# Optimization experiments

Hardware: AMD Instinct MI355X
Metric: run time of the kernel (lower is better)

## Reference

```python
import jax, jax.numpy as jnp
import numpy as np

HEADS = 16
DIM_HEAD = 64
QUERY_DIM = 1024
CONTEXT_DIM = 768
INNER = HEADS * DIM_HEAD  # 1024
SCALE = DIM_HEAD ** -0.5


def setup_inputs() -> dict:
    key = jax.random.key(0)
    ks = jax.random.split(key, 7)
    B, Sq, Skv = 4, 2048, 2048
    x = jax.random.normal(ks[0], (B, Sq, QUERY_DIM), dtype=jnp.float32)
    context = jax.random.normal(ks[1], (B, Skv, CONTEXT_DIM), dtype=jnp.float32)
    # Linear weights stored as (in, out) so y = x @ W
    w_q = jax.random.normal(ks[2], (QUERY_DIM, INNER), dtype=jnp.float32) / np.sqrt(QUERY_DIM)
    w_k = jax.random.normal(ks[3], (CONTEXT_DIM, INNER), dtype=jnp.float32) / np.sqrt(CONTEXT_DIM)
    w_v = jax.random.normal(ks[4], (CONTEXT_DIM, INNER), dtype=jnp.float32) / np.sqrt(CONTEXT_DIM)
    w_o = jax.random.normal(ks[5], (INNER, QUERY_DIM), dtype=jnp.float32) / np.sqrt(INNER)
    b_o = jax.random.normal(ks[6], (QUERY_DIM,), dtype=jnp.float32) * 0.02
    return {"x": x, "context": context, "w_q": w_q, "w_k": w_k, "w_v": w_v, "w_o": w_o, "b_o": b_o}


def reference(x, context, w_q, w_k, w_v, w_o, b_o):
    B, Sq, _ = x.shape
    Skv = context.shape[1]
    # projections, split heads: [B, S, H, D] -> [B, H, S, D]
    q = (x @ w_q).reshape(B, Sq, HEADS, DIM_HEAD).transpose(0, 2, 1, 3)
    k = (context @ w_k).reshape(B, Skv, HEADS, DIM_HEAD).transpose(0, 2, 1, 3)
    v = (context @ w_v).reshape(B, Skv, HEADS, DIM_HEAD).transpose(0, 2, 1, 3)
    sim = jnp.einsum('bhid,bhjd->bhij', q, k) * SCALE
    attn = jax.nn.softmax(sim, axis=-1)
    out = jnp.einsum('bhij,bhjd->bhid', attn, v)
    out = out.transpose(0, 2, 1, 3).reshape(B, Sq, INNER)
    return out @ w_o + b_o
```

## Files before the change

kernel.cpp:

```cpp
#include <hip/hip_runtime.h>

typedef __bf16 bf16_t;
typedef __bf16 bf16x8 __attribute__((ext_vector_type(8)));
typedef __bf16 bf16x4 __attribute__((ext_vector_type(4)));
typedef __bf16 bf16x2 __attribute__((ext_vector_type(2)));
typedef float  f32x4  __attribute__((ext_vector_type(4)));
typedef float  f32x16 __attribute__((ext_vector_type(16)));
typedef int    i32x4  __attribute__((ext_vector_type(4)));

#define AS_G(p) ((const __attribute__((address_space(1))) void*)(p))
#define AS_L(p) ((__attribute__((address_space(3))) void*)(p))
#define GLD16(g, l) __builtin_amdgcn_global_load_lds(AS_G(g), AS_L(l), 16, 0, 0)

static __device__ __forceinline__ f32x4 mfma16(bf16x8 a, bf16x8 b, f32x4 c) {
  return __builtin_amdgcn_mfma_f32_16x16x32_bf16(a, b, c, 0, 0, 0);
}
static __device__ __forceinline__ f32x16 mfma32(bf16x8 a, bf16x8 b, f32x16 c) {
  return __builtin_amdgcn_mfma_f32_32x32x16_bf16(a, b, c, 0, 0, 0);
}
static __device__ __forceinline__ int pk2(float a, float b) {
  bf16x2 t; t[0] = (bf16_t)a; t[1] = (bf16_t)b;
  return __builtin_bit_cast(int, t);
}
static __device__ __forceinline__ bf16x8 mk8(int a, int b, int c, int d) {
  i32x4 v{a, b, c, d};
  return __builtin_bit_cast(bf16x8, v);
}
static __device__ __forceinline__ void pl32swap(int& x, int& y) {
  asm volatile("v_permlane32_swap_b32 %0, %1" : "+v"(x), "+v"(y));
}

__global__ __launch_bounds__(256) void cvt_all_k(const float* __restrict__ x,
                                                 bf16_t* __restrict__ xb,
                                                 const float* __restrict__ ctx,
                                                 bf16_t* __restrict__ cb,
                                                 long nx, long ntot) {
  long i = ((long)blockIdx.x * 256 + threadIdx.x) * 4;
  long step = (long)gridDim.x * 256 * 4;
  for (; i < ntot; i += step) {
    const float* src; bf16_t* dst; long off;
    if (i < nx) { src = x; dst = xb; off = i; }
    else        { src = ctx; dst = cb; off = i - nx; }
    float4 v = *(const float4*)(src + off);
    bf16x4 o;
    o[0] = (bf16_t)v.x; o[1] = (bf16_t)v.y; o[2] = (bf16_t)v.z; o[3] = (bf16_t)v.w;
    *(bf16x4*)(dst + off) = o;
  }
}

__global__ __launch_bounds__(256) void tcvt_all_k(
    const float* __restrict__ w0, const float* __restrict__ w1,
    const float* __restrict__ w2, const float* __restrict__ w3,
    bf16_t* __restrict__ t0, bf16_t* __restrict__ t1,
    bf16_t* __restrict__ t2, bf16_t* __restrict__ t3) {
  __shared__ float t[32][33];
  const int z = blockIdx.z;
  const float* W = (z == 0) ? w0 : (z == 1) ? w1 : (z == 2) ? w2 : w3;
  bf16_t* Wt = (z == 0) ? t0 : (z == 1) ? t1 : (z == 2) ? t2 : t3;
  const int K = (z == 1 || z == 2) ? 768 : 1024;
  const int N = 1024;
  int k0 = blockIdx.y << 5, n0 = blockIdx.x << 5;
  if (k0 >= K) return;
  int ti = threadIdx.x >> 3, tj = (threadIdx.x & 7) << 2;
  float4 v = *(const float4*)(W + (size_t)(k0 + ti) * N + n0 + tj);
  t[ti][tj] = v.x; t[ti][tj + 1] = v.y; t[ti][tj + 2] = v.z; t[ti][tj + 3] = v.w;
  __syncthreads();
  bf16x4 o;
  o[0] = (bf16_t)t[tj + 0][ti]; o[1] = (bf16_t)t[tj + 1][ti];
  o[2] = (bf16_t)t[tj + 2][ti]; o[3] = (bf16_t)t[tj + 3][ti];
  *(bf16x4*)(Wt + (size_t)(n0 + ti) * K + k0 + tj) = o;
}

template <int MODE>
__global__ __launch_bounds__(256, 3) void gemm_bt_k(
    const bf16_t* __restrict__ A, const bf16_t* __restrict__ Bt,
    void* __restrict__ Cout, void* __restrict__ Cout2,
    const float* __restrict__ bias, int N, int K, float oscale) {
  __shared__ __align__(16) char lA[16384];
  __shared__ __align__(16) char lB[16384];
  const int tid = threadIdx.x;
  const int lane = tid & 63;
  const int w = tid >> 6;
  const int wr = (w >> 1) << 6;
  const int wc = (w & 1) << 6;
  const long row0 = (long)blockIdx.x << 7;
  const long col0 = (long)blockIdx.y << 7;

  const int r_st = tid >> 3;
  const int cb_st = ((tid & 7) << 4) ^ ((r_st & 7) << 4);
  const char* pa = (const char*)(A + (row0 + r_st) * (long)K) + cb_st;
  const char* pb = (const char*)(Bt + (col0 + r_st) * (long)K) + cb_st;
  const long rowstep = (long)K * 64;
  char* la = lA + tid * 16;
  char* lb = lB + tid * 16;

  f32x4 acc[4][4];
#pragma unroll
  for (int m = 0; m < 4; m++)
#pragma unroll
    for (int n = 0; n < 4; n++) acc[m][n] = f32x4{0.f, 0.f, 0.f, 0.f};

  for (int k0 = 0; k0 < K; k0 += 64) {
    __syncthreads();
#pragma unroll
    for (int i = 0; i < 4; i++) {
      GLD16(pa + i * rowstep, la + i * 4096);
      GLD16(pb + i * rowstep, lb + i * 4096);
    }
    __syncthreads();
    pa += 128; pb += 128;
#pragma unroll
    for (int ks = 0; ks < 2; ks++) {
      bf16x8 af[4], bfr[4];
#pragma unroll
      for (int m = 0; m < 4; m++) {
        int row = wr + (m << 4) + (lane & 15);
        int cby = ((ks << 6) + ((lane >> 4) << 4)) ^ ((row & 7) << 4);
        af[m] = *(const bf16x8*)(lA + row * 128 + cby);
      }
#pragma unroll
      for (int n = 0; n < 4; n++) {
        int row = wc + (n << 4) + (lane & 15);
        int cby = ((ks << 6) + ((lane >> 4) << 4)) ^ ((row & 7) << 4);
        bfr[n] = *(const bf16x8*)(lB + row * 128 + cby);
      }
      __builtin_amdgcn_s_setprio(1);
#pragma unroll
      for (int m = 0; m < 4; m++)
#pragma unroll
        for (int n = 0; n < 4; n++)
          acc[m][n] = mfma16(af[m], bfr[n], acc[m][n]);
      __builtin_amdgcn_s_setprio(0);
    }
  }

  if (MODE == 0) {
    bf16_t* Cb = (bf16_t*)Cout;
#pragma unroll
    for (int n = 0; n < 4; n++) {
      long c = col0 + wc + (n << 4) + (lane & 15);
      long h = c >> 6, d = c & 63;
#pragma unroll
      for (int m = 0; m < 4; m++) {
#pragma unroll
        for (int j = 0; j < 4; j++) {
          long rr = row0 + wr + (m << 4) + ((lane >> 4) << 2) + j;
          long bb = rr >> 11, s = rr & 2047;
          Cb[(((bb << 4) + h) * 2048 + s) * 64 + d] = (bf16_t)(acc[m][n][j] * oscale);
        }
      }
    }
  } else if (MODE == 1) {
    float* Cf = (float*)Cout;
#pragma unroll
    for (int n = 0; n < 4; n++) {
      long c = col0 + wc + (n << 4) + (lane & 15);
      float bv = bias[c];
#pragma unroll
      for (int m = 0; m < 4; m++) {
#pragma unroll
        for (int j = 0; j < 4; j++) {
          long rr = row0 + wr + (m << 4) + ((lane >> 4) << 2) + j;
          Cf[rr * (long)N + c] = acc[m][n][j] + bv;
        }
      }
    }
  } else {
    if (col0 < 1024) {
      bf16_t* Cb = (bf16_t*)Cout;
#pragma unroll
      for (int n = 0; n < 4; n++) {
        long c = col0 + wc + (n << 4) + (lane & 15);
        long h = c >> 6, d = c & 63;
#pragma unroll
        for (int m = 0; m < 4; m++) {
#pragma unroll
          for (int j = 0; j < 4; j++) {
            long rr = row0 + wr + (m << 4) + ((lane >> 4) << 2) + j;
            long bb = rr >> 11, s = rr & 2047;
            Cb[(((bb << 4) + h) * 2048 + s) * 64 + d] = (bf16_t)acc[m][n][j];
          }
        }
      }
    } else {
      bf16_t* Cb = (bf16_t*)Cout2;
#pragma unroll
      for (int n = 0; n < 4; n++) {
        long c = (col0 - 1024) + wc + (n << 4) + (lane & 15);
        long h = c >> 6, d = c & 63;
#pragma unroll
        for (int m = 0; m < 4; m++) {
          long rr = row0 + wr + (m << 4) + ((lane >> 4) << 2);
          long bb = rr >> 11, s = rr & 2047;
          bf16x4 ov;
#pragma unroll
          for (int j = 0; j < 4; j++) ov[j] = (bf16_t)acc[m][n][j];
          *(bf16x4*)(Cb + (((bb << 4) + h) * 64 + d) * 2048 + s) = ov;
        }
      }
    }
  }
}

__global__ __launch_bounds__(256, 3) void attn5_k(
    const bf16_t* __restrict__ Q, const bf16_t* __restrict__ Kh,
    const bf16_t* __restrict__ VT, bf16_t* __restrict__ O) {
  __shared__ __align__(16) char lds_[32768];
  const int tid = threadIdx.x;
  const int lane = tid & 63;
  const int w = tid >> 6;
  const int hi = lane >> 5;
  const int lq = lane & 31;
  const int bh = blockIdx.x;
  const int b = bh >> 4, hh = bh & 15;
  const int q = (blockIdx.y << 7) + (w << 5) + lq;

  const bf16_t* qp = Q + ((size_t)bh * 2048 + q) * 64 + (hi << 3);
  bf16x8 qf[4];
#pragma unroll
  for (int s = 0; s < 4; s++) qf[s] = *(const bf16x8*)(qp + (s << 4));

  const bf16x8 onesf = mk8(0x3F803F80, 0x3F803F80, 0x3F803F80, 0x3F803F80);

  const int r_st = tid >> 3;
  const int csw = ((tid & 7) << 4) ^ ((r_st & 7) << 4);
  const char* pk = (const char*)Kh + (size_t)bh * 262144 + r_st * 128 + csw;
  const char* pv = (const char*)VT + (size_t)bh * 262144 + (size_t)r_st * 4096 + csw;
  const int swz = (lane & 7) << 4;

  f32x16 oa[2], la;
#pragma unroll
  for (int t = 0; t < 2; t++)
#pragma unroll
    for (int r = 0; r < 16; r++) oa[t][r] = 0.f;
#pragma unroll
  for (int r = 0; r < 16; r++) la[r] = 0.f;

  GLD16(pk, lds_ + tid * 16);
  GLD16(pk + 4096, lds_ + 4096 + tid * 16);
  GLD16(pv, lds_ + 8192 + tid * 16);
  GLD16(pv + 131072, lds_ + 12288 + tid * 16);
  __syncthreads();

  for (int it = 0; it < 32; it++) {
    const int buf = it & 1;
    if (it < 31) {
      const char* pkn = pk + (it + 1) * 8192;
      const char* pvn = pv + (it + 1) * 128;
      char* dst = lds_ + ((buf ^ 1) << 14);
      GLD16(pkn, dst + tid * 16);
      GLD16(pkn + 4096, dst + 4096 + tid * 16);
      GLD16(pvn, dst + 8192 + tid * 16);
      GLD16(pvn + 131072, dst + 12288 + tid * 16);
    }
    const char* lk = lds_ + (buf << 14);
    const char* lv = lk + 8192;

    f32x16 sa[2];
#pragma unroll
    for (int h = 0; h < 2; h++) {
#pragma unroll
      for (int r = 0; r < 16; r++) sa[h][r] = 0.f;
      const char* krow = lk + (((h << 5) + lq) << 7);
      __builtin_amdgcn_s_setprio(1);
#pragma unroll
      for (int s = 0; s < 4; s++) {
        bf16x8 kf = *(const bf16x8*)(krow + (((s << 5) + (hi << 4)) ^ swz));
        sa[h] = mfma32(kf, qf[s], sa[h]);
      }
      __builtin_amdgcn_s_setprio(0);
    }

#pragma unroll
    for (int h = 0; h < 2; h++)
#pragma unroll
      for (int r = 0; r < 16; r++)
        sa[h][r] = __builtin_amdgcn_exp2f(sa[h][r]);

    bf16x8 pf[4];
#pragma unroll
    for (int h = 0; h < 2; h++) {
      int x0 = pk2(sa[h][0], sa[h][1]),   y0 = pk2(sa[h][4], sa[h][5]);
      int x1 = pk2(sa[h][2], sa[h][3]),   y1 = pk2(sa[h][6], sa[h][7]);
      pl32swap(x0, y0); pl32swap(x1, y1);
      pf[h * 2 + 0] = mk8(x0, x1, y0, y1);
      int x2 = pk2(sa[h][8], sa[h][9]),   y2 = pk2(sa[h][12], sa[h][13]);
      int x3 = pk2(sa[h][10], sa[h][11]), y3 = pk2(sa[h][14], sa[h][15]);
      pl32swap(x2, y2); pl32swap(x3, y3);
      pf[h * 2 + 1] = mk8(x2, x3, y2, y3);
    }

    __builtin_amdgcn_s_setprio(1);
#pragma unroll
    for (int t = 0; t < 2; t++) {
      const char* vrw = lv + (((t << 5) + lq) << 7);
#pragma unroll
      for (int s = 0; s < 4; s++) {
        bf16x8 vf = *(const bf16x8*)(vrw + (((s << 5) + (hi << 4)) ^ swz));
        oa[t] = mfma32(vf, pf[s], oa[t]);
      }
    }
#pragma unroll
    for (int s = 0; s < 4; s++) la = mfma32(onesf, pf[s], la);
    __builtin_amdgcn_s_setprio(0);
    __syncthreads();
  }

  float invl = 1.f / la[0];
  bf16_t* Ob = O + ((size_t)b * 2048 + q) * 1024 + hh * 64;
#pragma unroll
  for (int t = 0; t < 2; t++)
#pragma unroll
    for (int g = 0; g < 4; g++) {
      bf16x4 ov;
#pragma unroll
      for (int j = 0; j < 4; j++) ov[j] = (bf16_t)(oa[t][(g << 2) + j] * invl);
      *(bf16x4*)(Ob + (t << 5) + (g << 3) + (hi << 2)) = ov;
    }
}

extern "C" void kernel_launch(void* const* d_in, const int* in_sizes, int n_in,
                              void* d_out, int out_size, void* d_ws, size_t ws_size,
                              hipStream_t stream) {
  (void)in_sizes; (void)n_in; (void)out_size; (void)ws_size;
  const float* x   = (const float*)d_in[0];
  const float* ctx = (const float*)d_in[1];
  const float* w_q = (const float*)d_in[2];
  const float* w_k = (const float*)d_in[3];
  const float* w_v = (const float*)d_in[4];
  const float* w_o = (const float*)d_in[5];
  const float* b_o = (const float*)d_in[6];

  char* ws = (char*)d_ws;
  const size_t MB = 1 << 20;
  bf16_t* xb  = (bf16_t*)(ws);
  bf16_t* cb  = (bf16_t*)(ws + 16 * MB);
  bf16_t* wqT = (bf16_t*)(ws + 28 * MB);
  bf16_t* wkT = (bf16_t*)(ws + 30 * MB);
  bf16_t* wvT = (bf16_t*)(ws + 31 * MB + 512 * 1024);
  bf16_t* woT = (bf16_t*)(ws + 33 * MB);
  bf16_t* qws = (bf16_t*)(ws + 35 * MB);
  bf16_t* kws = (bf16_t*)(ws + 51 * MB);
  bf16_t* vtw = (bf16_t*)(ws + 67 * MB);
  bf16_t* ows = xb;

  cvt_all_k<<<2048, 256, 0, stream>>>(x, xb, ctx, cb, 8388608L, 14680064L);
  tcvt_all_k<<<dim3(32, 32, 4), 256, 0, stream>>>(w_q, w_k, w_v, w_o, wqT, wkT, wvT, woT);

  const float qs = 0.125f * 1.4426950408889634f;
  gemm_bt_k<0><<<dim3(64, 8), 256, 0, stream>>>(xb, wqT, qws, nullptr, nullptr, 1024, 1024, qs);
  gemm_bt_k<3><<<dim3(64, 16), 256, 0, stream>>>(cb, wkT, kws, vtw, nullptr, 2048, 768, 1.0f);
  attn5_k<<<dim3(64, 16), 256, 0, stream>>>(qws, kws, vtw, ows);
  gemm_bt_k<1><<<dim3(64, 8), 256, 0, stream>>>(ows, woT, d_out, nullptr, b_o, 1024, 1024, 1.0f);
}
```

Measured before the change: 172.0 us.

## Fuse fp32-to-bf16 activation conversion into projection GEMM A-tile loads

Removes the standalone conversion kernel for x and context. The Q and KV projection GEMMs now read fp32 activations directly into registers, convert them to bf16 and write them swizzled into LDS, with the next tile prefetched in registers. This saves a kernel launch and a full write and re-read of the bf16 activation copies. In exchange the A operand uses register-staged loads instead of async global-to-LDS loads, which raises register pressure and reads twice the bytes per tile. Under the Q/KV grids each row of x or context is also read and converted once per column block instead of once overall.

```diff
diff --git a/kernel.cpp b/kernel.cpp
--- a/kernel.cpp
+++ b/kernel.cpp
@@ -28,24 +28,6 @@
 }
 static __device__ __forceinline__ void pl32swap(int& x, int& y) {
   asm volatile("v_permlane32_swap_b32 %0, %1" : "+v"(x), "+v"(y));
-}
-
-__global__ __launch_bounds__(256) void cvt_all_k(const float* __restrict__ x,
-                                                 bf16_t* __restrict__ xb,
-                                                 const float* __restrict__ ctx,
-                                                 bf16_t* __restrict__ cb,
-                                                 long nx, long ntot) {
-  long i = ((long)blockIdx.x * 256 + threadIdx.x) * 4;
-  long step = (long)gridDim.x * 256 * 4;
-  for (; i < ntot; i += step) {
-    const float* src; bf16_t* dst; long off;
-    if (i < nx) { src = x; dst = xb; off = i; }
-    else        { src = ctx; dst = cb; off = i - nx; }
-    float4 v = *(const float4*)(src + off);
-    bf16x4 o;
-    o[0] = (bf16_t)v.x; o[1] = (bf16_t)v.y; o[2] = (bf16_t)v.z; o[3] = (bf16_t)v.w;
-    *(bf16x4*)(dst + off) = o;
-  }
 }
 
 __global__ __launch_bounds__(256) void tcvt_all_k(
@@ -71,9 +53,9 @@
   *(bf16x4*)(Wt + (size_t)(n0 + ti) * K + k0 + tj) = o;
 }
 
-template <int MODE>
+template <int MODE, int AF32>
 __global__ __launch_bounds__(256, 3) void gemm_bt_k(
-    const bf16_t* __restrict__ A, const bf16_t* __restrict__ Bt,
+    const void* __restrict__ Ain, const bf16_t* __restrict__ Bt,
     void* __restrict__ Cout, void* __restrict__ Cout2,
     const float* __restrict__ bias, int N, int K, float oscale) {
   __shared__ __align__(16) char lA[16384];
@@ -88,27 +70,54 @@
 
   const int r_st = tid >> 3;
   const int cb_st = ((tid & 7) << 4) ^ ((r_st & 7) << 4);
-  const char* pa = (const char*)(A + (row0 + r_st) * (long)K) + cb_st;
   const char* pb = (const char*)(Bt + (col0 + r_st) * (long)K) + cb_st;
   const long rowstep = (long)K * 64;
   char* la = lA + tid * 16;
   char* lb = lB + tid * 16;
 
+  const char* pa = (const char*)((const bf16_t*)Ain + (row0 + r_st) * (long)K) + cb_st;
+  const float* paf = (const float*)Ain + (row0 + (tid >> 1)) * (long)K + ((tid & 1) << 5);
+  char* lwa = lA + (tid >> 1) * 128;
+  const int hb = (tid & 1) << 6;
+  const int rsw = ((tid >> 1) & 7) << 4;
+
   f32x4 acc[4][4];
 #pragma unroll
   for (int m = 0; m < 4; m++)
 #pragma unroll
     for (int n = 0; n < 4; n++) acc[m][n] = f32x4{0.f, 0.f, 0.f, 0.f};
+
+  float4 av[8];
+  if (AF32) {
+#pragma unroll
+    for (int i = 0; i < 8; i++) av[i] = *(const float4*)(paf + (i << 2));
+    paf += 64;
+  }
 
   for (int k0 = 0; k0 < K; k0 += 64) {
     __syncthreads();
 #pragma unroll
-    for (int i = 0; i < 4; i++) {
-      GLD16(pa + i * rowstep, la + i * 4096);
-      GLD16(pb + i * rowstep, lb + i * 4096);
+    for (int i = 0; i < 4; i++) GLD16(pb + i * rowstep, lb + i * 4096);
+    if (AF32) {
+#pragma unroll
+      for (int i = 0; i < 4; i++) {
+        i32x4 wv{pk2(av[2 * i].x, av[2 * i].y), pk2(av[2 * i].z, av[2 * i].w),
+                 pk2(av[2 * i + 1].x, av[2 * i + 1].y),
+                 pk2(av[2 * i + 1].z, av[2 * i + 1].w)};
+        *(i32x4*)(lwa + ((hb + (i << 4)) ^ rsw)) = wv;
+      }
+    } else {
+#pragma unroll
+      for (int i = 0; i < 4; i++) GLD16(pa + i * rowstep, la + i * 4096);
+      pa += 128;
     }
     __syncthreads();
-    pa += 128; pb += 128;
+    pb += 128;
+    if (AF32 && k0 + 64 < K) {
+#pragma unroll
+      for (int i = 0; i < 8; i++) av[i] = *(const float4*)(paf + (i << 2));
+      paf += 64;
+    }
 #pragma unroll
     for (int ks = 0; ks < 2; ks++) {
       bf16x8 af[4], bfr[4];
@@ -333,8 +342,7 @@
 
   char* ws = (char*)d_ws;
   const size_t MB = 1 << 20;
-  bf16_t* xb  = (bf16_t*)(ws);
-  bf16_t* cb  = (bf16_t*)(ws + 16 * MB);
+  bf16_t* ows = (bf16_t*)(ws);
   bf16_t* wqT = (bf16_t*)(ws + 28 * MB);
   bf16_t* wkT = (bf16_t*)(ws + 30 * MB);
   bf16_t* wvT = (bf16_t*)(ws + 31 * MB + 512 * 1024);
@@ -342,14 +350,12 @@
   bf16_t* qws = (bf16_t*)(ws + 35 * MB);
   bf16_t* kws = (bf16_t*)(ws + 51 * MB);
   bf16_t* vtw = (bf16_t*)(ws + 67 * MB);
-  bf16_t* ows = xb;
-
-  cvt_all_k<<<2048, 256, 0, stream>>>(x, xb, ctx, cb, 8388608L, 14680064L);
+
   tcvt_all_k<<<dim3(32, 32, 4), 256, 0, stream>>>(w_q, w_k, w_v, w_o, wqT, wkT, wvT, woT);
 
   const float qs = 0.125f * 1.4426950408889634f;
-  gemm_bt_k<0><<<dim3(64, 8), 256, 0, stream>>>(xb, wqT, qws, nullptr, nullptr, 1024, 1024, qs);
-  gemm_bt_k<3><<<dim3(64, 16), 256, 0, stream>>>(cb, wkT, kws, vtw, nullptr, 2048, 768, 1.0f);
+  gemm_bt_k<0, 1><<<dim3(64, 8), 256, 0, stream>>>(x, wqT, qws, nullptr, nullptr, 1024, 1024, qs);
+  gemm_bt_k<3, 1><<<dim3(64, 16), 256, 0, stream>>>(ctx, wkT, kws, vtw, nullptr, 2048, 768, 1.0f);
   attn5_k<<<dim3(64, 16), 256, 0, stream>>>(qws, kws, vtw, ows);
-  gemm_bt_k<1><<<dim3(64, 8), 256, 0, stream>>>(ows, woT, d_out, nullptr, b_o, 1024, 1024, 1.0f);
-}
+  gemm_bt_k<1, 0><<<dim3(64, 8), 256, 0, stream>>>(ows, woT, d_out, nullptr, b_o, 1024, 1024, 1.0f);
+}
```

New measurement: 211.9 us. +23.2%, slower.
